# Optimization experiments

Hardware: AMD Instinct MI355X
Metric: run time of the kernel (lower is better)

Reference implementation:

```python
import jax, jax.numpy as jnp
import numpy as np

D_MODEL = 1024
N_HEADS = 16
HEAD_DIM = D_MODEL // N_HEADS


def setup_inputs() -> dict:
    key = jax.random.key(0)
    ks = jax.random.split(key, 9)
    B, T, S, D = 4, 2048, 512, D_MODEL
    sc = 1.0 / np.sqrt(D)
    return {
        "x": jax.random.normal(ks[0], (B, T, D), dtype=jnp.float32),
        "context": jax.random.normal(ks[1], (B, S, D), dtype=jnp.float32),
        "context_mask": jnp.ones((B, S), dtype=bool),
        "Wq": jax.random.normal(ks[2], (D, D), dtype=jnp.float32) * sc,
        "bq": jnp.zeros((D,), dtype=jnp.float32),
        "Wkv": jax.random.normal(ks[3], (D, 2 * D), dtype=jnp.float32) * sc,
        "bkv": jnp.zeros((2 * D,), dtype=jnp.float32),
        "Wp": jax.random.normal(ks[4], (D, D), dtype=jnp.float32) * sc,
        "bp": jnp.zeros((D,), dtype=jnp.float32),
    }


def reference(x, context, context_mask, Wq, bq, Wkv, bkv, Wp, bp):
    B, T, D = x.shape
    S = context.shape[1]
    H, Hd = N_HEADS, HEAD_DIM
    # projections
    q = (x @ Wq + bq).reshape(B, T, H, Hd).transpose(0, 2, 1, 3)          # [B,H,T,Hd]
    kv = (context @ Wkv + bkv).reshape(B, S, 2, H, Hd)
    k = kv[:, :, 0].transpose(0, 2, 1, 3)                                  # [B,H,S,Hd]
    v = kv[:, :, 1].transpose(0, 2, 1, 3)                                  # [B,H,S,Hd]
    # scaled dot-product attention with context mask
    scores = jnp.einsum("bhtd,bhsd->bhts", q, k) / np.sqrt(Hd)            # [B,H,T,S]
    neg_inf = jnp.finfo(scores.dtype).min
    scores = jnp.where(context_mask[:, None, None, :], scores, neg_inf)
    attn = jax.nn.softmax(scores, axis=-1)
    # dropout is identity in eval mode (p applied only in training)
    out = jnp.einsum("bhts,bhsd->bthd", attn, v).reshape(B, T, D)
    return out @ Wp + bp
```

## Files before the change

kernel.cpp:

```cpp
#include <hip/hip_runtime.h>

typedef __bf16 bf16x8 __attribute__((ext_vector_type(8)));
typedef float  f32x4  __attribute__((ext_vector_type(4)));

#define MFMA(a, b, c) __builtin_amdgcn_mfma_f32_16x16x32_bf16((a), (b), (c), 0, 0, 0)

#define GLL(g, l) __builtin_amdgcn_global_load_lds(                                  \
    (const __attribute__((address_space(1))) void*)(g),                              \
    (__attribute__((address_space(3))) void*)(l), 16, 0, 0)

#define BB 4
#define TT 2048
#define SS 512
#define DM 1024
#define NH 16
#define HD 64

__device__ __forceinline__ unsigned short f2b(float f) {
    union { float f; unsigned int u; } v; v.f = f;
    unsigned int r = (v.u + 0x7fffu + ((v.u >> 16) & 1u)) >> 16;
    return (unsigned short)r;
}
__device__ __forceinline__ unsigned short f2bh(float f) {
    __bf16 h = (__bf16)f;
    union { __bf16 h; unsigned short u; } v; v.h = h;
    return v.u;
}

__device__ __forceinline__ void tcast_tile(const float* __restrict__ in,
                                           unsigned short* __restrict__ out,
                                           int K, int N, int n0, int k0,
                                           float (*tile)[33], int tid) {
    int tx = tid & 31, ty = tid >> 5;
#pragma unroll
    for (int r = 0; r < 32; r += 8)
        tile[ty + r][tx] = in[(k0 + ty + r) * N + n0 + tx];
    __syncthreads();
#pragma unroll
    for (int r = 0; r < 32; r += 8)
        out[(n0 + ty + r) * K + k0 + tx] = f2b(tile[tx][ty + r]);
}

__global__ __launch_bounds__(256)
void prep(const float4* __restrict__ x, const float4* __restrict__ ctx,
          const unsigned int* __restrict__ mw,
          const float* __restrict__ Wq, const float* __restrict__ Wkv,
          const float* __restrict__ Wp,
          ushort4* __restrict__ Xbf, ushort4* __restrict__ Cbf,
          unsigned short* __restrict__ WqT, unsigned short* __restrict__ WkvT,
          unsigned short* __restrict__ WpT, float* __restrict__ mbias) {
    __shared__ float tile[32][33];
    __shared__ int flags[2];
    const int bid = blockIdx.x, tid = threadIdx.x;
    if (bid < 8192) {
        int i = bid * 256 + tid;
        float4 v = x[i];
        ushort4 o; o.x = f2b(v.x); o.y = f2b(v.y); o.z = f2b(v.z); o.w = f2b(v.w);
        Xbf[i] = o;
    } else if (bid < 10240) {
        int i = (bid - 8192) * 256 + tid;
        float4 v = ctx[i];
        ushort4 o; o.x = f2b(v.x); o.y = f2b(v.y); o.z = f2b(v.z); o.w = f2b(v.w);
        Cbf[i] = o;
    } else if (bid < 11264) {
        int loc = bid - 10240;
        tcast_tile(Wq, WqT, DM, DM, (loc & 31) * 32, (loc >> 5) * 32, tile, tid);
    } else if (bid < 13312) {
        int loc = bid - 11264;
        tcast_tile(Wkv, WkvT, DM, 2 * DM, (loc & 63) * 32, (loc >> 6) * 32, tile, tid);
    } else if (bid < 14336) {
        int loc = bid - 13312;
        tcast_tile(Wp, WpT, DM, DM, (loc & 31) * 32, (loc >> 5) * 32, tile, tid);
    } else {
        if (tid == 0) { flags[0] = 1; flags[1] = 1; }
        __syncthreads();
        int okI = 1, okF = 1;
        for (int i = tid; i < 512; i += 256) {
            unsigned int w = mw[i];
            if (w > 1u) okI = 0;
            if (w != 0u && w != 0x3f800000u) okF = 0;
        }
        if (!okI) atomicAnd(&flags[0], 0);
        if (!okF) atomicAnd(&flags[1], 0);
        __syncthreads();
        bool wordLayout = (flags[0] != 0) || (flags[1] != 0);
        const unsigned char* mb = (const unsigned char*)mw;
        for (int s = tid; s < BB * SS; s += 256) {
            bool on = wordLayout ? (mw[s] != 0u) : (mb[s] != 0);
            mbias[s] = on ? 0.0f : -1e38f;
        }
    }
}

__device__ __forceinline__ void gemm_core(
    const unsigned short* __restrict__ A, const unsigned short* __restrict__ Bt,
    int K, int m0, int n0, unsigned short* As, unsigned short* Bs,
    f32x4 (*acc)[4]) {
    const int tid = threadIdx.x;
    const int w = tid >> 6, l = tid & 63;
    const int quad = l >> 4, col = l & 15;
    const int wm = w * 64;
    const int arow = tid >> 3;
    const int apiece = (tid & 7) ^ (arow & 7);
    const unsigned short* Ab = A + (size_t)(m0 + arow) * K + apiece * 8;
    const unsigned short* Bb = Bt + (size_t)(n0 + arow) * K + apiece * 8;

    for (int k0 = 0; k0 < K; k0 += 64) {
        __syncthreads();
#pragma unroll
        for (int g = 0; g < 8; ++g)
            GLL(Ab + k0 + g * 16 * K, &As[g * 1024 + tid * 8]);
#pragma unroll
        for (int g = 0; g < 4; ++g)
            GLL(Bb + k0 + g * 16 * K, &Bs[g * 1024 + tid * 8]);
        __syncthreads();
#pragma unroll
        for (int k32 = 0; k32 < 2; ++k32) {
            bf16x8 af[4], bf[4];
#pragma unroll
            for (int i = 0; i < 4; i++) {
                int rr = wm + i * 16 + col;
                af[i] = *(const bf16x8*)&As[rr * 64 + (((k32 * 4 + quad) ^ (rr & 7)) * 8)];
            }
#pragma unroll
            for (int j = 0; j < 4; j++) {
                int rr = j * 16 + col;
                bf[j] = *(const bf16x8*)&Bs[rr * 64 + (((k32 * 4 + quad) ^ (rr & 7)) * 8)];
            }
#pragma unroll
            for (int i = 0; i < 4; i++)
#pragma unroll
                for (int j = 0; j < 4; j++) acc[i][j] = MFMA(af[i], bf[j], acc[i][j]);
        }
    }
}

__global__ __launch_bounds__(128, 3)
void gemm_qkv(const unsigned short* __restrict__ Xbf, const unsigned short* __restrict__ WqT,
              const float* __restrict__ bq, unsigned short* __restrict__ Qb,
              const unsigned short* __restrict__ Cbf, const unsigned short* __restrict__ WkvT,
              const float* __restrict__ bkv, unsigned short* __restrict__ Kb,
              unsigned short* __restrict__ Vtb) {
    __shared__ __align__(16) unsigned short As[128 * 64];
    __shared__ __align__(16) unsigned short Bs[64 * 64];
    const int tid = threadIdx.x;
    const int w = tid >> 6, l = tid & 63;
    const int quad = l >> 4, col = l & 15;
    const int bid = blockIdx.x;

    const f32x4 zero = {0.f, 0.f, 0.f, 0.f};
    f32x4 acc[4][4];
#pragma unroll
    for (int i = 0; i < 4; i++)
#pragma unroll
        for (int j = 0; j < 4; j++) acc[i][j] = zero;

    if (bid < 1024) {
        const int m0 = (bid >> 4) * 128, n0 = (bid & 15) * 64;
        gemm_core(Xbf, WqT, DM, m0, n0, As, Bs, acc);
        const float QS = 0.125f * 1.4426950408889634f;
#pragma unroll
        for (int i = 0; i < 4; i++) {
#pragma unroll
            for (int j = 0; j < 4; j++) {
                int n = n0 + j * 16 + col;
                int mb = m0 + w * 64 + i * 16 + quad * 4;
                float bv = bq[n];
#pragma unroll
                for (int ii = 0; ii < 4; ii++)
                    Qb[(mb + ii) * DM + n] = f2bh((acc[i][j][ii] + bv) * QS);
            }
        }
    } else {
        const int loc = bid - 1024;
        const int m0 = (loc >> 5) * 128, n0 = (loc & 31) * 64;
        gemm_core(Cbf, WkvT, DM, m0, n0, As, Bs, acc);
#pragma unroll
        for (int i = 0; i < 4; i++) {
#pragma unroll
            for (int j = 0; j < 4; j++) {
                int n = n0 + j * 16 + col;
                int mb = m0 + w * 64 + i * 16 + quad * 4;
                float bv = bkv[n];
                if (n < 1024) {
                    int h = n >> 6, d = n & 63;
#pragma unroll
                    for (int ii = 0; ii < 4; ii++) {
                        int m = mb + ii; int b = m >> 9, s = m & 511;
                        Kb[(((b * NH + h) * SS) + s) * HD + d] = f2bh(acc[i][j][ii] + bv);
                    }
                } else {
                    int q = n - 1024; int h = q >> 6, d = q & 63;
#pragma unroll
                    for (int ii = 0; ii < 4; ii++) {
                        int m = mb + ii; int b = m >> 9, s = m & 511;
                        Vtb[(((b * NH + h) * HD) + d) * SS + s] = f2bh(acc[i][j][ii] + bv);
                    }
                }
            }
        }
    }
}

__global__ __launch_bounds__(128, 3)
void gemm_out(const unsigned short* __restrict__ Ob, const unsigned short* __restrict__ WpT,
              const float* __restrict__ bp, float* __restrict__ out) {
    __shared__ __align__(16) unsigned short As[128 * 64];
    __shared__ __align__(16) unsigned short Bs[64 * 64];
    const int tid = threadIdx.x;
    const int w = tid >> 6, l = tid & 63;
    const int quad = l >> 4, col = l & 15;
    const int bid = blockIdx.x;
    const int m0 = (bid >> 4) * 128, n0 = (bid & 15) * 64;

    const f32x4 zero = {0.f, 0.f, 0.f, 0.f};
    f32x4 acc[4][4];
#pragma unroll
    for (int i = 0; i < 4; i++)
#pragma unroll
        for (int j = 0; j < 4; j++) acc[i][j] = zero;

    gemm_core(Ob, WpT, DM, m0, n0, As, Bs, acc);

#pragma unroll
    for (int i = 0; i < 4; i++) {
#pragma unroll
        for (int j = 0; j < 4; j++) {
            int n = n0 + j * 16 + col;
            int mb = m0 + w * 64 + i * 16 + quad * 4;
            float bv = bp[n];
#pragma unroll
            for (int ii = 0; ii < 4; ii++)
                out[(mb + ii) * DM + n] = acc[i][j][ii] + bv;
        }
    }
}

__global__ __launch_bounds__(512, 4)
void flash_attn(const unsigned short* __restrict__ Q, const unsigned short* __restrict__ Kb,
                const unsigned short* __restrict__ Vt, const float* __restrict__ mbias,
                unsigned short* __restrict__ O) {
    const int bid = blockIdx.x;
    const int tb = bid & 7, bh = bid >> 3;
    const int b = bh >> 4;
    const int tid = threadIdx.x;
    const int w = tid >> 6, l = tid & 63;
    const int quad = l >> 4, col = l & 15;

    __shared__ __align__(16) unsigned short Ks[2][64 * 64];
    __shared__ __align__(16) unsigned short Vs[2][64 * 64];
    __shared__ __align__(16) unsigned short Pb[8][32 * 40];
    __shared__ float biasS[SS];

    const unsigned short* Kh = Kb + bh * SS * HD;
    const unsigned short* Vh = Vt + bh * HD * SS;

    biasS[tid] = mbias[b * SS + tid];

    const int rowbase = b * TT + tb * 256 + w * 32;
    bf16x8 qf[2][2];
#pragma unroll
    for (int rg = 0; rg < 2; rg++) {
        const unsigned short* qrow = Q + (rowbase + rg * 16 + col) * DM + (bh & 15) * HD;
        qf[rg][0] = *(const bf16x8*)(qrow + quad * 8);
        qf[rg][1] = *(const bf16x8*)(qrow + 32 + quad * 8);
    }

    const int sr = tid >> 3, sp = tid & 7;
    const int spk = ((sp ^ (sr & 7)) * 8);
    const int kgo = sr * HD + spk;
    const int vgo = sr * SS + spk;

    GLL(Kh + kgo, &Ks[0][tid * 8]);
    GLL(Vh + vgo, &Vs[0][tid * 8]);

    const f32x4 zero = {0.f, 0.f, 0.f, 0.f};
    f32x4 o[2][4];
#pragma unroll
    for (int rg = 0; rg < 2; rg++)
#pragma unroll
        for (int j = 0; j < 4; j++) o[rg][j] = zero;
    f32x4 lsum[2] = {zero, zero};

    for (int it = 0; it < SS / 64; ++it) {
        const int s0 = it * 64;
        const int buf = it & 1;
        __syncthreads();
        if (it + 1 < SS / 64) {
            GLL(Kh + (s0 + 64) * HD + kgo, &Ks[buf ^ 1][tid * 8]);
            GLL(Vh + (s0 + 64) + vgo, &Vs[buf ^ 1][tid * 8]);
        }

#pragma unroll
        for (int h2 = 0; h2 < 2; ++h2) {
            f32x4 sc[2][2];
#pragma unroll
            for (int jj = 0; jj < 2; ++jj) {
                int row = (2 * h2 + jj) * 16 + col;
                bf16x8 k0 = *(const bf16x8*)&Ks[buf][row * 64 + ((quad ^ (row & 7)) * 8)];
                bf16x8 k1 = *(const bf16x8*)&Ks[buf][row * 64 + (((4 + quad) ^ (row & 7)) * 8)];
#pragma unroll
                for (int rg = 0; rg < 2; rg++) {
                    f32x4 t = MFMA(qf[rg][0], k0, zero);
                    sc[rg][jj] = MFMA(qf[rg][1], k1, t);
                }
            }
#pragma unroll
            for (int rg = 0; rg < 2; rg++) {
#pragma unroll
                for (int jj = 0; jj < 2; jj++) {
                    float bb = biasS[s0 + (2 * h2 + jj) * 16 + col];
#pragma unroll
                    for (int i = 0; i < 4; i++) {
                        float p = exp2f(sc[rg][jj][i] + bb);
                        lsum[rg][i] += p;
                        Pb[w][(rg * 16 + quad * 4 + i) * 40 + jj * 16 + col] = f2bh(p);
                    }
                }
            }
            asm volatile("s_waitcnt lgkmcnt(0)" ::: "memory");
            bf16x8 pf[2];
#pragma unroll
            for (int rg = 0; rg < 2; rg++)
                pf[rg] = *(const bf16x8*)&Pb[w][(rg * 16 + col) * 40 + quad * 8];
#pragma unroll
            for (int j2 = 0; j2 < 4; j2++) {
                int row = j2 * 16 + col;
                bf16x8 vf = *(const bf16x8*)&Vs[buf][row * 64 + (((h2 * 4 + quad) ^ (row & 7)) * 8)];
#pragma unroll
                for (int rg = 0; rg < 2; rg++)
                    o[rg][j2] = MFMA(pf[rg], vf, o[rg][j2]);
            }
            asm volatile("" ::: "memory");
        }
    }

#pragma unroll
    for (int rg = 0; rg < 2; rg++) {
#pragma unroll
        for (int i = 0; i < 4; i++) {
            float rs = lsum[rg][i];
#pragma unroll
            for (int off = 1; off < 16; off <<= 1) rs += __shfl_xor(rs, off);
            float inv = 1.0f / rs;
            unsigned short* orow = O + (rowbase + rg * 16 + quad * 4 + i) * DM
                                     + (bh & 15) * HD + col;
#pragma unroll
            for (int j2 = 0; j2 < 4; j2++)
                orow[j2 * 16] = f2bh(o[rg][j2][i] * inv);
        }
    }
}

extern "C" void kernel_launch(void* const* d_in, const int* in_sizes, int n_in,
                              void* d_out, int out_size, void* d_ws, size_t ws_size,
                              hipStream_t stream) {
    const float* x    = (const float*)d_in[0];
    const float* ctx  = (const float*)d_in[1];
    const void*  cmsk = d_in[2];
    const float* Wq   = (const float*)d_in[3];
    const float* bq   = (const float*)d_in[4];
    const float* Wkv  = (const float*)d_in[5];
    const float* bkv  = (const float*)d_in[6];
    const float* Wp   = (const float*)d_in[7];
    const float* bp   = (const float*)d_in[8];
    float* out = (float*)d_out;

    char* ws = (char*)d_ws;
    size_t off = 0;
    auto alloc = [&](size_t bytes) -> void* {
        void* p = ws + off;
        off += (bytes + 255) & ~(size_t)255;
        return p;
    };
    const size_t NX = (size_t)BB * TT * DM;
    const size_t NC = (size_t)BB * SS * DM;
    unsigned short* Xbf  = (unsigned short*)alloc(NX * 2);
    unsigned short* Cbf  = (unsigned short*)alloc(NC * 2);
    unsigned short* WqT  = (unsigned short*)alloc((size_t)DM * DM * 2);
    unsigned short* WkvT = (unsigned short*)alloc((size_t)DM * 2 * DM * 2);
    unsigned short* WpT  = (unsigned short*)alloc((size_t)DM * DM * 2);
    unsigned short* Qb   = (unsigned short*)alloc(NX * 2);
    unsigned short* Kbf  = (unsigned short*)alloc(NC * 2);
    unsigned short* Vtb  = (unsigned short*)alloc(NC * 2);
    unsigned short* Ob   = (unsigned short*)alloc(NX * 2);
    float* mbias         = (float*)alloc((size_t)BB * SS * 4);

    prep<<<14337, 256, 0, stream>>>((const float4*)x, (const float4*)ctx,
                                    (const unsigned int*)cmsk, Wq, Wkv, Wp,
                                    (ushort4*)Xbf, (ushort4*)Cbf,
                                    WqT, WkvT, WpT, mbias);

    gemm_qkv<<<1536, 128, 0, stream>>>(Xbf, WqT, bq, Qb, Cbf, WkvT, bkv, Kbf, Vtb);

    flash_attn<<<BB * NH * (TT / 256), 512, 0, stream>>>(Qb, Kbf, Vtb, mbias, Ob);

    gemm_out<<<1024, 128, 0, stream>>>(Ob, WpT, bp, out);
}
```

Measured before the change: 214.2 us.

## Remap block indices to XCD-aware order and vectorize weight transpose-cast stores

Block IDs in the projection GEMMs, output GEMM and flash attention are remapped so that blocks landing on the same XCD (bid mod 8) share the same weight columns or K/V heads, which should improve L2 reuse across the chiplets. The weight transpose-cast now writes four bf16 values per thread with one ushort4 store instead of four scalar stores. The manual round-to-nearest bf16 conversion is replaced by the compiler's native __bf16 cast, which may use a hardware convert instruction. These change the block schedule and store pattern, and may add LDS bank conflicts in the transpose read.

```diff
diff --git a/kernel.cpp b/kernel.cpp
--- a/kernel.cpp
+++ b/kernel.cpp
@@ -16,11 +16,6 @@
 #define NH 16
 #define HD 64
 
-__device__ __forceinline__ unsigned short f2b(float f) {
-    union { float f; unsigned int u; } v; v.f = f;
-    unsigned int r = (v.u + 0x7fffu + ((v.u >> 16) & 1u)) >> 16;
-    return (unsigned short)r;
-}
 __device__ __forceinline__ unsigned short f2bh(float f) {
     __bf16 h = (__bf16)f;
     union { __bf16 h; unsigned short u; } v; v.h = h;
@@ -36,9 +31,13 @@
     for (int r = 0; r < 32; r += 8)
         tile[ty + r][tx] = in[(k0 + ty + r) * N + n0 + tx];
     __syncthreads();
-#pragma unroll
-    for (int r = 0; r < 32; r += 8)
-        out[(n0 + ty + r) * K + k0 + tx] = f2b(tile[tx][ty + r]);
+    int r2 = tid >> 3, cg = (tid & 7) * 4;
+    ushort4 o;
+    o.x = f2bh(tile[cg + 0][r2]);
+    o.y = f2bh(tile[cg + 1][r2]);
+    o.z = f2bh(tile[cg + 2][r2]);
+    o.w = f2bh(tile[cg + 3][r2]);
+    *(ushort4*)&out[(n0 + r2) * K + k0 + cg] = o;
 }
 
 __global__ __launch_bounds__(256)
@@ -55,12 +54,12 @@
     if (bid < 8192) {
         int i = bid * 256 + tid;
         float4 v = x[i];
-        ushort4 o; o.x = f2b(v.x); o.y = f2b(v.y); o.z = f2b(v.z); o.w = f2b(v.w);
+        ushort4 o; o.x = f2bh(v.x); o.y = f2bh(v.y); o.z = f2bh(v.z); o.w = f2bh(v.w);
         Xbf[i] = o;
     } else if (bid < 10240) {
         int i = (bid - 8192) * 256 + tid;
         float4 v = ctx[i];
-        ushort4 o; o.x = f2b(v.x); o.y = f2b(v.y); o.z = f2b(v.z); o.w = f2b(v.w);
+        ushort4 o; o.x = f2bh(v.x); o.y = f2bh(v.y); o.z = f2bh(v.z); o.w = f2bh(v.w);
         Cbf[i] = o;
     } else if (bid < 11264) {
         int loc = bid - 10240;
@@ -156,7 +155,9 @@
         for (int j = 0; j < 4; j++) acc[i][j] = zero;
 
     if (bid < 1024) {
-        const int m0 = (bid >> 4) * 128, n0 = (bid & 15) * 64;
+        const int xg = bid & 7, t = bid >> 3;
+        const int m0 = (xg + 8 * (t & 7)) * 128;
+        const int n0 = (t >> 3) * 64;
         gemm_core(Xbf, WqT, DM, m0, n0, As, Bs, acc);
         const float QS = 0.125f * 1.4426950408889634f;
 #pragma unroll
@@ -173,7 +174,9 @@
         }
     } else {
         const int loc = bid - 1024;
-        const int m0 = (loc >> 5) * 128, n0 = (loc & 31) * 64;
+        const int xg = loc & 7, t = loc >> 3;
+        const int m0 = (xg + 8 * (t & 1)) * 128;
+        const int n0 = (t >> 1) * 64;
         gemm_core(Cbf, WkvT, DM, m0, n0, As, Bs, acc);
 #pragma unroll
         for (int i = 0; i < 4; i++) {
@@ -211,7 +214,9 @@
     const int w = tid >> 6, l = tid & 63;
     const int quad = l >> 4, col = l & 15;
     const int bid = blockIdx.x;
-    const int m0 = (bid >> 4) * 128, n0 = (bid & 15) * 64;
+    const int xg = bid & 7, t = bid >> 3;
+    const int m0 = (xg + 8 * (t & 7)) * 128;
+    const int n0 = (t >> 3) * 64;
 
     const f32x4 zero = {0.f, 0.f, 0.f, 0.f};
     f32x4 acc[4][4];
@@ -241,7 +246,9 @@
                 const unsigned short* __restrict__ Vt, const float* __restrict__ mbias,
                 unsigned short* __restrict__ O) {
     const int bid = blockIdx.x;
-    const int tb = bid & 7, bh = bid >> 3;
+    const int xg = bid & 7, tq = bid >> 3;
+    const int tb = tq & 7;
+    const int bh = xg + 8 * (tq >> 3);
     const int b = bh >> 4;
     const int tid = threadIdx.x;
     const int w = tid >> 6, l = tid & 63;
@@ -301,8 +308,8 @@
                 bf16x8 k1 = *(const bf16x8*)&Ks[buf][row * 64 + (((4 + quad) ^ (row & 7)) * 8)];
 #pragma unroll
                 for (int rg = 0; rg < 2; rg++) {
-                    f32x4 t = MFMA(qf[rg][0], k0, zero);
-                    sc[rg][jj] = MFMA(qf[rg][1], k1, t);
+                    f32x4 tt = MFMA(qf[rg][0], k0, zero);
+                    sc[rg][jj] = MFMA(qf[rg][1], k1, tt);
                 }
             }
 #pragma unroll
```

Result: faster. 209.5 us (-2.2%).
